# Optimization experiments

Measured on AMD Instinct MI355X. Metric: run time of the kernel, lower is better.

## Reference

```python
import jax, jax.numpy as jnp
import numpy as np

B, S, DIM, SDIM = 4, 4096, 1024, 256


def setup_inputs() -> dict:
    key = jax.random.key(0)
    ks = jax.random.split(key, 10)
    def lin(k, din, dout):
        return jax.random.normal(k, (din, dout), jnp.float32) / np.float32(np.sqrt(din))
    return {
        "x": jax.random.normal(ks[0], (B, S, DIM), jnp.float32),
        "ln_g": jnp.ones((DIM,), jnp.float32),
        "ln_b": jnp.zeros((DIM,), jnp.float32),
        "mix_w": jax.random.normal(ks[1], (DIM, 1, 3), jnp.float32) * 0.3,  # depthwise conv kernel
        "mix_b": jnp.zeros((DIM,), jnp.float32),
        "Wi": lin(ks[2], DIM, DIM), "bi": jnp.zeros((DIM,), jnp.float32),
        "Wsin": lin(ks[3], DIM, SDIM), "bsin": jnp.zeros((SDIM,), jnp.float32),
        "Wd": lin(ks[4], DIM, SDIM), "bd": jnp.zeros((SDIM,), jnp.float32),
        "Wsel": lin(ks[5], DIM, SDIM), "bsel": jnp.zeros((SDIM,), jnp.float32),
        "Wso": lin(ks[6], SDIM, DIM), "bso": jnp.zeros((DIM,), jnp.float32),
        "Wg": lin(ks[7], DIM, DIM), "bg": jnp.zeros((DIM,), jnp.float32),
        "Wout": lin(ks[8], DIM, DIM), "bout": jnp.zeros((DIM,), jnp.float32),
    }


def reference(x, ln_g, ln_b, mix_w, mix_b, Wi, bi, Wsin, bsin, Wd, bd,
              Wsel, bsel, Wso, bso, Wg, bg, Wout, bout):
    eps = 1e-5
    # LayerNorm over last dim
    mu = jnp.mean(x, axis=-1, keepdims=True)
    var = jnp.mean(jnp.square(x - mu), axis=-1, keepdims=True)
    h = (x - mu) * jax.lax.rsqrt(var + eps) * ln_g + ln_b
    # depthwise Conv1d, kernel=3, padding=1, groups=dim
    hc = jnp.transpose(h, (0, 2, 1))  # [B, C, L]
    mixed = jax.lax.conv_general_dilated(
        hc, mix_w, window_strides=(1,), padding=[(1, 1)],
        dimension_numbers=("NCH", "OIH", "NCH"), feature_group_count=hc.shape[1])
    mixed = jnp.transpose(mixed + mix_b[None, :, None], (0, 2, 1))  # [B, S, D]
    u = jnp.tanh(mixed @ Wi + bi)                 # [B, S, D]
    x_state = jnp.tanh(mixed @ Wsin + bsin)       # [B, S, N]
    decay = jax.nn.sigmoid(mixed @ Wd + bd)       # [B, S, N]
    select = jax.nn.sigmoid(mixed @ Wsel + bsel)  # [B, S, N]
    # sequential linear recurrence: state = d*state + (1-d)*x_state
    def step(state, inp):
        dt, xt = inp
        state = dt * state + (1.0 - dt) * xt
        return state, state
    init = jnp.zeros((x.shape[0], x_state.shape[-1]), x.dtype)
    _, states = jax.lax.scan(step, init,
                             (jnp.swapaxes(decay, 0, 1), jnp.swapaxes(x_state, 0, 1)))
    states = jnp.swapaxes(states, 0, 1)           # [B, S, N]
    y = (select * states) @ Wso + bso             # [B, S, D]
    g = jax.nn.sigmoid(mixed @ Wg + bg)
    out = (g * y + (1.0 - g) * u) @ Wout + bout
    return x + out
```

## Files before the change

### kernel.cpp

```cpp
#include <hip/hip_runtime.h>
#include <hip/hip_bf16.h>
#include <math.h>

typedef __bf16 bf16_t;
typedef __bf16 bf16x8 __attribute__((ext_vector_type(8)));
typedef __bf16 bf16x4 __attribute__((ext_vector_type(4)));
typedef float  f32x4  __attribute__((ext_vector_type(4)));

#define B_ 4
#define S_ 4096
#define D_ 1024
#define N_ 256
#define M_ (B_*S_)

__device__ __forceinline__ float fsig(float x){
    return __builtin_amdgcn_rcpf(1.0f + __expf(-x));
}
__device__ __forceinline__ float ftanh(float x){
    return 1.0f - 2.0f*__builtin_amdgcn_rcpf(1.0f + __expf(2.0f*x));
}

__device__ __forceinline__ void gload_lds16(const void* g, void* l){
    __builtin_amdgcn_global_load_lds(
        (const __attribute__((address_space(1))) unsigned int*)g,
        (__attribute__((address_space(3))) unsigned int*)l, 16, 0, 0);
}

struct TJobs {
    const float* in[7];
    bf16_t*      out[7];
    int R[7];
    int C[7];
};

__global__ void transpose_all(TJobs j){
    int z = blockIdx.z;
    int R = j.R[z], C = j.C[z];
    int c0 = blockIdx.x*32, r0 = blockIdx.y*32;
    if (c0 >= C || r0 >= R) return;
    __shared__ float tile[32][33];
    int tx = threadIdx.x, ty = threadIdx.y;
    const float* in = j.in[z];
    bf16_t* out = j.out[z];
    #pragma unroll
    for (int i=0;i<32;i+=8)
        tile[ty+i][tx] = in[(size_t)(r0+ty+i)*C + (c0+tx)];
    __syncthreads();
    #pragma unroll
    for (int i=0;i<32;i+=8)
        out[(size_t)(c0+ty+i)*R + (r0+tx)] = (bf16_t)tile[tx][ty+i];
}

__global__ void ln_kernel(const float* __restrict__ x, const float* __restrict__ gw,
                          const float* __restrict__ bw, bf16_t* __restrict__ h){
    int row = blockIdx.x;
    int t = threadIdx.x;
    float4 v = ((const float4*)(x + (size_t)row*D_))[t];
    float s = v.x+v.y+v.z+v.w;
    float q = v.x*v.x+v.y*v.y+v.z*v.z+v.w*v.w;
    #pragma unroll
    for (int o=1;o<64;o<<=1){ s += __shfl_xor(s,o,64); q += __shfl_xor(q,o,64); }
    __shared__ float sw[4], sq[4];
    int wid = t>>6;
    if ((t&63)==0){ sw[wid]=s; sq[wid]=q; }
    __syncthreads();
    s = sw[0]+sw[1]+sw[2]+sw[3];
    q = sq[0]+sq[1]+sq[2]+sq[3];
    float mu = s*(1.0f/D_);
    float rs = rsqrtf(q*(1.0f/D_) - mu*mu + 1e-5f);
    float4 gv = ((const float4*)gw)[t];
    float4 bv = ((const float4*)bw)[t];
    bf16x4 o4;
    o4[0] = (bf16_t)((v.x-mu)*rs*gv.x + bv.x);
    o4[1] = (bf16_t)((v.y-mu)*rs*gv.y + bv.y);
    o4[2] = (bf16_t)((v.z-mu)*rs*gv.z + bv.z);
    o4[3] = (bf16_t)((v.w-mu)*rs*gv.w + bv.w);
    *(bf16x4*)(h + (size_t)row*D_ + t*4) = o4;
}

__global__ void conv_kernel(const bf16_t* __restrict__ h, const float* __restrict__ w,
                            const float* __restrict__ mb, bf16_t* __restrict__ mix){
    int idx = blockIdx.x*256 + threadIdx.x;
    int g8  = idx & 127;
    int row = idx >> 7;
    int s   = row & (S_-1);
    int d0  = g8*8;
    const bf16_t* hr = h + (size_t)row*D_ + d0;
    bf16x8 cur = *(const bf16x8*)hr;
    bf16x8 prv, nxt;
    #pragma unroll
    for (int i=0;i<8;i++){ prv[i]=(bf16_t)0.0f; nxt[i]=(bf16_t)0.0f; }
    if (s > 0)      prv = *(const bf16x8*)(hr - D_);
    if (s < S_-1)   nxt = *(const bf16x8*)(hr + D_);
    bf16x8 ov;
    #pragma unroll
    for (int i=0;i<8;i++){
        int d = d0+i;
        float o = (float)prv[i]*w[d*3] + (float)cur[i]*w[d*3+1] + (float)nxt[i]*w[d*3+2] + mb[d];
        ov[i] = (bf16_t)o;
    }
    *(bf16x8*)(mix + (size_t)row*D_ + d0) = ov;
}

struct Epi {
    const float *b0,*b1,*b2,*b3,*b4;
    bf16_t *u, *g, *z;
    bf16_t *xs, *dc, *sel;
    const bf16_t *gbuf, *ubuf;
    const float *resid;
    float *outp;
};

#define WAITV4()  asm volatile("s_waitcnt vmcnt(4)" ::: "memory")
#define WAITV0()  asm volatile("s_waitcnt vmcnt(0)" ::: "memory")
#define WAITLGK0() asm volatile("s_waitcnt lgkmcnt(0)" ::: "memory")
#define CFENCE()  asm volatile("" ::: "memory")
#define BARR()    __builtin_amdgcn_s_barrier()

template<int MODE>
__global__ __launch_bounds__(512,2)
void gemm256(const bf16_t* __restrict__ A, const bf16_t* __restrict__ Bt,
             int K, Epi e){
    extern __shared__ __align__(16) char lds[];
    const int TILE = 16384;
    int t = threadIdx.x;
    int wave = t>>6, lane = t&63;
    int wm = (wave>>2)*128;
    int wn = (wave&3)*64;
    int lm = lane&15, quad = lane>>4;
    int m0 = blockIdx.x*256, n0 = blockIdx.y*256;
    int NT = K>>5;

    int srow = t>>2;
    int scol = (t&3)*8;
    const bf16_t* gA = A  + (size_t)(m0+srow)*K + scol;
    const bf16_t* gB = Bt + (size_t)(n0+srow)*K + scol;

    auto stage = [&](int kt, int buf){
        const bf16_t* a = gA + kt*32;
        const bf16_t* b = gB + kt*32;
        char* da = lds + buf*TILE + t*16;
        char* db = lds + 32768 + buf*TILE + t*16;
        gload_lds16(a,                  da);
        gload_lds16(a + (size_t)128*K,  da + 8192);
        gload_lds16(b,                  db);
        gload_lds16(b + (size_t)128*K,  db + 8192);
    };

    int raBase = (wm+lm)*64 + quad*16;
    int rbBase = (wn+lm)*64 + quad*16;

    f32x4 acc[8][4];
    #pragma unroll
    for (int i=0;i<8;i++)
        #pragma unroll
        for (int j=0;j<4;j++)
            #pragma unroll
            for (int r=0;r<4;r++) acc[i][j][r]=0.0f;

    bf16x8 aF[8], bF[4];

    stage(0,0);
    stage(1,1);
    WAITV4();
    BARR();
    CFENCE();

    for (int kt=0; kt<NT; ++kt){
        int buf = kt&1;
        const char* pa = lds + buf*TILE + raBase;
        const char* pb = lds + 32768 + buf*TILE + rbBase;

        #pragma unroll
        for (int j=0;j<4;j++) bF[j] = *(const bf16x8*)(pb + j*1024);
        #pragma unroll
        for (int i=0;i<8;i++) aF[i] = *(const bf16x8*)(pa + i*1024);

        __builtin_amdgcn_s_setprio(1);
        #pragma unroll
        for (int i=0;i<8;i++)
            #pragma unroll
            for (int j=0;j<4;j++)
                acc[i][j] = __builtin_amdgcn_mfma_f32_16x16x32_bf16(aF[i], bF[j], acc[i][j], 0,0,0);
        __builtin_amdgcn_s_setprio(0);

        WAITLGK0();
        BARR();
        CFENCE();
        if (kt+2 < NT){
            stage(kt+2, buf);
            WAITV4();
            BARR();
            CFENCE();
        } else if (kt+1 < NT){
            WAITV0();
            BARR();
            CFENCE();
        }
    }
    __syncthreads();

    if (MODE==0 || MODE==1){
        const float* bp = e.b0; int cbase = 0; bf16_t* dst = 0; int width = D_;
        bool ut = true;
        if (MODE==0){
            ut = (n0 < 1280);
            if (n0 < 1024){ bp=e.b0; cbase=n0; dst=e.u; width=D_; }
            else if (n0 < 1792){
                int sub=(n0-1024)>>8;
                bp  = sub==0? e.b1 : sub==1? e.b2 : e.b3;
                dst = sub==0? e.xs : sub==1? e.dc : e.sel;
                cbase = 0; width = N_;
            } else { bp=e.b4; cbase=n0-1792; dst=e.g; width=D_; }
        } else {
            bp = e.b0; cbase = n0; width = D_;
        }
        bf16_t* Tb = (bf16_t*)lds;
        #pragma unroll
        for (int h=0; h<4; h++){
            if (h) __syncthreads();
            if (wm == (h>>1)*128){
                int ib = (h&1)*4;
                #pragma unroll
                for (int ii=0;ii<4;ii++){
                    #pragma unroll
                    for (int j=0;j<4;j++){
                        float bv = bp[(MODE==0?cbase:n0) + wn + j*16 + lm];
                        #pragma unroll
                        for (int r=0;r<4;r++){
                            float v = acc[ib+ii][j][r] + bv;
                            if (MODE==0) v = ut ? ftanh(v) : fsig(v);
                            Tb[(ii*16+quad*4+r)*264 + wn + j*16 + lm] = (bf16_t)v;
                        }
                    }
                }
            }
            __syncthreads();
            if (MODE==0){
                #pragma unroll
                for (int it=0; it<4; it++){
                    int idx = it*512 + t;
                    int row = idx>>5, c8 = idx&31;
                    bf16x8 v = *(const bf16x8*)&Tb[row*264 + c8*8];
                    *(bf16x8*)&dst[(size_t)(m0 + h*64 + row)*width + cbase + c8*8] = v;
                }
            } else {
                #pragma unroll
                for (int it=0; it<4; it++){
                    int idx = it*512 + t;
                    int row = idx>>5, c8 = idx&31;
                    bf16x8 y = *(const bf16x8*)&Tb[row*264 + c8*8];
                    size_t gi = (size_t)(m0 + h*64 + row)*D_ + n0 + c8*8;
                    bf16x8 gv = *(const bf16x8*)&e.gbuf[gi];
                    bf16x8 uv = *(const bf16x8*)&e.ubuf[gi];
                    bf16x8 o;
                    #pragma unroll
                    for (int q=0;q<8;q++){
                        float gf = (float)gv[q];
                        o[q] = (bf16_t)(gf*(float)y[q] + (1.0f-gf)*(float)uv[q]);
                    }
                    *(bf16x8*)&e.z[gi] = o;
                }
            }
        }
    } else {
        float* T = (float*)lds;
        #pragma unroll
        for (int pZ=0; pZ<8; pZ++){
            if (pZ) __syncthreads();
            if (wm == (pZ>>2)*128){
                int ib = (pZ&3)*2;
                #pragma unroll
                for (int ii=0;ii<2;ii++){
                    #pragma unroll
                    for (int j=0;j<4;j++)
                        #pragma unroll
                        for (int r=0;r<4;r++)
                            T[(ii*16+quad*4+r)*260 + wn + j*16 + lm] = acc[ib+ii][j][r];
                }
            }
            __syncthreads();
            #pragma unroll
            for (int it=0; it<4; it++){
                int idx = it*512 + t;
                int row = idx>>6, c4 = idx&63;
                f32x4 v = *(const f32x4*)&T[row*260 + c4*4];
                size_t gi = (size_t)(m0 + pZ*32 + row)*D_ + n0 + c4*4;
                float4 res = *(const float4*)&e.resid[gi];
                float4 bb  = *(const float4*)&e.b0[n0 + c4*4];
                float4 o;
                o.x = v[0]+res.x+bb.x; o.y = v[1]+res.y+bb.y;
                o.z = v[2]+res.z+bb.z; o.w = v[3]+res.w+bb.w;
                *(float4*)&e.outp[gi] = o;
            }
        }
    }
}

__global__ void scan_p1(const bf16_t* __restrict__ dc, const bf16_t* __restrict__ xs,
                        float* __restrict__ aggA, float* __restrict__ aggB){
    int bc = blockIdx.x;
    int b = bc>>6, ch = bc&63;
    int n = threadIdx.x;
    size_t base = ((size_t)b*S_ + ch*64)*N_ + n;
    float A = 1.0f, Bc = 0.0f;
    for (int t=0;t<64;t++){
        float d = (float)dc[base + (size_t)t*N_];
        float x = (float)xs[base + (size_t)t*N_];
        A  = d*A;
        Bc = d*Bc + (1.0f-d)*x;
    }
    aggA[(size_t)bc*N_+n]=A; aggB[(size_t)bc*N_+n]=Bc;
}

__global__ void scan_p2(const float* __restrict__ aggA, const float* __restrict__ aggB,
                        float* __restrict__ pre){
    int b = blockIdx.x, n = threadIdx.x;
    float s = 0.0f;
    for (int ch=0; ch<64; ch++){
        size_t i = ((size_t)b*64+ch)*N_+n;
        pre[i] = s;
        s = aggA[i]*s + aggB[i];
    }
}

__global__ void scan_p3(const bf16_t* __restrict__ dc, const bf16_t* __restrict__ xs,
                        const bf16_t* __restrict__ sel, const float* __restrict__ pre,
                        bf16_t* __restrict__ ss){
    int bc = blockIdx.x;
    int b = bc>>6, ch = bc&63;
    int n = threadIdx.x;
    size_t base = ((size_t)b*S_ + ch*64)*N_ + n;
    float s = pre[(size_t)bc*N_+n];
    for (int t=0;t<64;t++){
        size_t i = base + (size_t)t*N_;
        float d = (float)dc[i], x = (float)xs[i];
        s = d*s + (1.0f-d)*x;
        ss[i] = (bf16_t)((float)sel[i]*s);
    }
}

extern "C" void kernel_launch(void* const* d_in, const int* in_sizes, int n_in,
                              void* d_out, int out_size, void* d_ws, size_t ws_size,
                              hipStream_t stream){
    const float* x    = (const float*)d_in[0];
    const float* ln_g = (const float*)d_in[1];
    const float* ln_b = (const float*)d_in[2];
    const float* mixw = (const float*)d_in[3];
    const float* mixb = (const float*)d_in[4];
    const float* Wi   = (const float*)d_in[5];
    const float* bi   = (const float*)d_in[6];
    const float* Wsin = (const float*)d_in[7];
    const float* bsin = (const float*)d_in[8];
    const float* Wd   = (const float*)d_in[9];
    const float* bd   = (const float*)d_in[10];
    const float* Wsel = (const float*)d_in[11];
    const float* bsel = (const float*)d_in[12];
    const float* Wso  = (const float*)d_in[13];
    const float* bso  = (const float*)d_in[14];
    const float* Wg   = (const float*)d_in[15];
    const float* bg   = (const float*)d_in[16];
    const float* Wout = (const float*)d_in[17];
    const float* bout = (const float*)d_in[18];
    float* out = (float*)d_out;

    char* p = (char*)d_ws;
    auto alloc = [&](size_t bytes)->char*{ char* r=p; p += (bytes+255)&~(size_t)255; return r; };
    bf16_t* hB    = (bf16_t*)alloc((size_t)M_*D_*2);
    bf16_t* mixB  = (bf16_t*)alloc((size_t)M_*D_*2);
    bf16_t* uB    = (bf16_t*)alloc((size_t)M_*D_*2);
    bf16_t* gB    = (bf16_t*)alloc((size_t)M_*D_*2);
    bf16_t* ssB   = (bf16_t*)alloc((size_t)M_*N_*2);
    bf16_t* xs    = (bf16_t*)alloc((size_t)M_*N_*2);
    bf16_t* dc    = (bf16_t*)alloc((size_t)M_*N_*2);
    bf16_t* sel   = (bf16_t*)alloc((size_t)M_*N_*2);
    bf16_t* WbigT = (bf16_t*)alloc((size_t)2816*1024*2);
    bf16_t* WsoT  = (bf16_t*)alloc(1024*256*2);
    bf16_t* WoutT = (bf16_t*)alloc(1024*1024*2);
    float*  aggA  = (float*)alloc((size_t)4*64*256*4);
    float*  aggB  = (float*)alloc((size_t)4*64*256*4);
    float*  pre   = (float*)alloc((size_t)4*64*256*4);
    bf16_t* zB = mixB;

    TJobs tj;
    tj.in[0]=Wi;   tj.out[0]=WbigT;            tj.R[0]=1024; tj.C[0]=1024;
    tj.in[1]=Wsin; tj.out[1]=WbigT+1024*1024;  tj.R[1]=1024; tj.C[1]=256;
    tj.in[2]=Wd;   tj.out[2]=WbigT+1280*1024;  tj.R[2]=1024; tj.C[2]=256;
    tj.in[3]=Wsel; tj.out[3]=WbigT+1536*1024;  tj.R[3]=1024; tj.C[3]=256;
    tj.in[4]=Wg;   tj.out[4]=WbigT+(size_t)1792*1024; tj.R[4]=1024; tj.C[4]=1024;
    tj.in[5]=Wso;  tj.out[5]=WsoT;             tj.R[5]=256;  tj.C[5]=1024;
    tj.in[6]=Wout; tj.out[6]=WoutT;            tj.R[6]=1024; tj.C[6]=1024;
    transpose_all<<<dim3(32,32,7), dim3(32,8), 0, stream>>>(tj);

    ln_kernel  <<<M_, 256, 0, stream>>>(x, ln_g, ln_b, hB);
    conv_kernel<<<M_*128/256, 256, 0, stream>>>(hB, mixw, mixb, mixB);

    Epi e0 = {};
    e0.b0=bi; e0.b1=bsin; e0.b2=bd; e0.b3=bsel; e0.b4=bg;
    e0.u=uB; e0.g=gB; e0.xs=xs; e0.dc=dc; e0.sel=sel;
    gemm256<0><<<dim3(M_/256, 11), 512, 65536, stream>>>(mixB, WbigT, 1024, e0);

    scan_p1<<<4*64, 256, 0, stream>>>(dc, xs, aggA, aggB);
    scan_p2<<<4,    256, 0, stream>>>(aggA, aggB, pre);
    scan_p3<<<4*64, 256, 0, stream>>>(dc, xs, sel, pre, ssB);

    Epi e1 = {};
    e1.b0=bso; e1.gbuf=gB; e1.ubuf=uB; e1.z=zB;
    gemm256<1><<<dim3(M_/256, 4), 512, 65536, stream>>>(ssB, WsoT, 256, e1);

    Epi e2 = {};
    e2.b0=bout; e2.resid=x; e2.outp=out;
    gemm256<2><<<dim3(M_/256, 4), 512, 65536, stream>>>(zB, WoutT, 1024, e2);
}
```

Measured before the change: 415.4 us.

## Shrink GEMM tiles to 128x256 with swizzled block mapping and higher occupancy

All three GEMMs now use a 128x256 output tile instead of 256x256, which halves the A-tile LDS footprint and the accumulator registers and raises launch bounds to allow four blocks per CU. Block indices are remapped with an 8-way interleave so neighbouring workgroups share A/B panels in cache. The s_setprio hints around the MFMA loop are removed. The change doubles the grid size, aiming at better CU fill and latency hiding, at the cost of more B-tile reloads and lower arithmetic intensity per block.

```diff
diff --git a/kernel.cpp b/kernel.cpp
--- a/kernel.cpp
+++ b/kernel.cpp
@@ -111,85 +111,86 @@
     float *outp;
 };
 
-#define WAITV4()  asm volatile("s_waitcnt vmcnt(4)" ::: "memory")
+#define WAITV3()  asm volatile("s_waitcnt vmcnt(3)" ::: "memory")
 #define WAITV0()  asm volatile("s_waitcnt vmcnt(0)" ::: "memory")
 #define WAITLGK0() asm volatile("s_waitcnt lgkmcnt(0)" ::: "memory")
 #define CFENCE()  asm volatile("" ::: "memory")
 #define BARR()    __builtin_amdgcn_s_barrier()
 
 template<int MODE>
-__global__ __launch_bounds__(512,2)
-void gemm256(const bf16_t* __restrict__ A, const bf16_t* __restrict__ Bt,
+__global__ __launch_bounds__(512,4)
+void gemm128(const bf16_t* __restrict__ A, const bf16_t* __restrict__ Bt,
              int K, Epi e){
     extern __shared__ __align__(16) char lds[];
-    const int TILE = 16384;
+    const int ATILE = 8192;
+    const int BTILE = 16384;
     int t = threadIdx.x;
     int wave = t>>6, lane = t&63;
-    int wm = (wave>>2)*128;
+    int wm = (wave>>2)*64;
     int wn = (wave&3)*64;
     int lm = lane&15, quad = lane>>4;
-    int m0 = blockIdx.x*256, n0 = blockIdx.y*256;
+
+    int flat = blockIdx.y*gridDim.x + blockIdx.x;
+    int nwg  = gridDim.x*gridDim.y;
+    int wg   = (flat&7)*(nwg>>3) + (flat>>3);
+    int m0 = (wg & 127)*128;
+    int n0 = (wg >> 7)*256;
     int NT = K>>5;
 
-    int srow = t>>2;
-    int scol = (t&3)*8;
-    const bf16_t* gA = A  + (size_t)(m0+srow)*K + scol;
-    const bf16_t* gB = Bt + (size_t)(n0+srow)*K + scol;
+    const bf16_t* gA = A  + (size_t)(m0 + (t>>2))*K + (t&3)*8;
+    const bf16_t* gB = Bt + (size_t)(n0 + (t>>2))*K + (t&3)*8;
 
     auto stage = [&](int kt, int buf){
         const bf16_t* a = gA + kt*32;
         const bf16_t* b = gB + kt*32;
-        char* da = lds + buf*TILE + t*16;
-        char* db = lds + 32768 + buf*TILE + t*16;
-        gload_lds16(a,                  da);
-        gload_lds16(a + (size_t)128*K,  da + 8192);
-        gload_lds16(b,                  db);
-        gload_lds16(b + (size_t)128*K,  db + 8192);
+        char* da = lds + buf*ATILE + t*16;
+        char* db = lds + 16384 + buf*BTILE + t*16;
+        gload_lds16(a, da);
+        gload_lds16(b, db);
+        gload_lds16(b + (size_t)128*K, db + 8192);
     };
 
     int raBase = (wm+lm)*64 + quad*16;
     int rbBase = (wn+lm)*64 + quad*16;
 
-    f32x4 acc[8][4];
-    #pragma unroll
-    for (int i=0;i<8;i++)
+    f32x4 acc[4][4];
+    #pragma unroll
+    for (int i=0;i<4;i++)
         #pragma unroll
         for (int j=0;j<4;j++)
             #pragma unroll
             for (int r=0;r<4;r++) acc[i][j][r]=0.0f;
 
-    bf16x8 aF[8], bF[4];
+    bf16x8 aF[4], bF[4];
 
     stage(0,0);
     stage(1,1);
-    WAITV4();
+    WAITV3();
     BARR();
     CFENCE();
 
     for (int kt=0; kt<NT; ++kt){
         int buf = kt&1;
-        const char* pa = lds + buf*TILE + raBase;
-        const char* pb = lds + 32768 + buf*TILE + rbBase;
+        const char* pa = lds + buf*ATILE + raBase;
+        const char* pb = lds + 16384 + buf*BTILE + rbBase;
 
         #pragma unroll
         for (int j=0;j<4;j++) bF[j] = *(const bf16x8*)(pb + j*1024);
         #pragma unroll
-        for (int i=0;i<8;i++) aF[i] = *(const bf16x8*)(pa + i*1024);
-
-        __builtin_amdgcn_s_setprio(1);
-        #pragma unroll
-        for (int i=0;i<8;i++)
+        for (int i=0;i<4;i++) aF[i] = *(const bf16x8*)(pa + i*1024);
+
+        #pragma unroll
+        for (int i=0;i<4;i++)
             #pragma unroll
             for (int j=0;j<4;j++)
                 acc[i][j] = __builtin_amdgcn_mfma_f32_16x16x32_bf16(aF[i], bF[j], acc[i][j], 0,0,0);
-        __builtin_amdgcn_s_setprio(0);
 
         WAITLGK0();
         BARR();
         CFENCE();
         if (kt+2 < NT){
             stage(kt+2, buf);
-            WAITV4();
+            WAITV3();
             BARR();
             CFENCE();
         } else if (kt+1 < NT){
@@ -217,10 +218,9 @@
         }
         bf16_t* Tb = (bf16_t*)lds;
         #pragma unroll
-        for (int h=0; h<4; h++){
+        for (int h=0; h<2; h++){
             if (h) __syncthreads();
-            if (wm == (h>>1)*128){
-                int ib = (h&1)*4;
+            if (wm == h*64){
                 #pragma unroll
                 for (int ii=0;ii<4;ii++){
                     #pragma unroll
@@ -228,7 +228,7 @@
                         float bv = bp[(MODE==0?cbase:n0) + wn + j*16 + lm];
                         #pragma unroll
                         for (int r=0;r<4;r++){
-                            float v = acc[ib+ii][j][r] + bv;
+                            float v = acc[ii][j][r] + bv;
                             if (MODE==0) v = ut ? ftanh(v) : fsig(v);
                             Tb[(ii*16+quad*4+r)*264 + wn + j*16 + lm] = (bf16_t)v;
                         }
@@ -266,10 +266,10 @@
     } else {
         float* T = (float*)lds;
         #pragma unroll
-        for (int pZ=0; pZ<8; pZ++){
+        for (int pZ=0; pZ<4; pZ++){
             if (pZ) __syncthreads();
-            if (wm == (pZ>>2)*128){
-                int ib = (pZ&3)*2;
+            if (wm == (pZ>>1)*64){
+                int ib = (pZ&1)*2;
                 #pragma unroll
                 for (int ii=0;ii<2;ii++){
                     #pragma unroll
@@ -398,7 +398,7 @@
     Epi e0 = {};
     e0.b0=bi; e0.b1=bsin; e0.b2=bd; e0.b3=bsel; e0.b4=bg;
     e0.u=uB; e0.g=gB; e0.xs=xs; e0.dc=dc; e0.sel=sel;
-    gemm256<0><<<dim3(M_/256, 11), 512, 65536, stream>>>(mixB, WbigT, 1024, e0);
+    gemm128<0><<<dim3(M_/128, 11), 512, 49152, stream>>>(mixB, WbigT, 1024, e0);
 
     scan_p1<<<4*64, 256, 0, stream>>>(dc, xs, aggA, aggB);
     scan_p2<<<4,    256, 0, stream>>>(aggA, aggB, pre);
@@ -406,9 +406,9 @@
 
     Epi e1 = {};
     e1.b0=bso; e1.gbuf=gB; e1.ubuf=uB; e1.z=zB;
-    gemm256<1><<<dim3(M_/256, 4), 512, 65536, stream>>>(ssB, WsoT, 256, e1);
+    gemm128<1><<<dim3(M_/128, 4), 512, 49152, stream>>>(ssB, WsoT, 256, e1);
 
     Epi e2 = {};
     e2.b0=bout; e2.resid=x; e2.outp=out;
-    gemm256<2><<<dim3(M_/256, 4), 512, 65536, stream>>>(zB, WoutT, 1024, e2);
-}
+    gemm128<2><<<dim3(M_/128, 4), 512, 49152, stream>>>(zB, WoutT, 1024, e2);
+}
```

After: 404.7 us. 1.03x faster.
